# Performance work log

Measured on AMD Instinct MI355X. Metric: run time of the kernel, lower is better.

## Reference

```python
import jax, jax.numpy as jnp
import numpy as np

E = 64        # num_local_experts
N = 32768     # total permuted tokens
H = 1024      # hidden_dim
F = 1024      # intermediate_dim
C = N // E    # per-expert capacity (setup uses equal token counts)


def setup_inputs() -> dict:
    key = jax.random.key(0)
    k1, k2, k3, k4 = jax.random.split(key, 4)
    s = 0.02  # init scale
    return {
        "permuted_local_hidden_states": jax.random.normal(k1, (N, H), jnp.float32),
        "tokens_per_expert": jnp.full((E,), C, dtype=jnp.int32),
        "w_gate": jax.random.normal(k2, (E, H, F), jnp.float32) * s,
        "w_up": jax.random.normal(k3, (E, H, F), jnp.float32) * s,
        "w_down": jax.random.normal(k4, (E, F, H), jnp.float32) * s,
    }


def reference(permuted_local_hidden_states, tokens_per_expert, w_gate, w_up, w_down):
    x = permuted_local_hidden_states  # [N, H], sorted by expert
    counts = tokens_per_expert.astype(jnp.int32)  # [E]
    # start offset of each expert's contiguous token range (torch cumsum + cat([0]))
    starts = jnp.concatenate([jnp.zeros((1,), jnp.int32), jnp.cumsum(counts)])[:-1]
    # expert id and within-expert position for every token (jit-friendly dispatch)
    eid = jnp.repeat(jnp.arange(E, dtype=jnp.int32), counts, total_repeat_length=N)
    pos = jnp.arange(N, dtype=jnp.int32) - starts[eid]
    # gather tokens into fixed-capacity per-expert buffer [E, C, H]; unused slots stay 0
    buf = jnp.zeros((E, C, H), x.dtype).at[eid, pos].set(x)
    # grouped LLaMA MLP: down( silu(gate(x)) * up(x) ), one GEMM triple per expert, batched
    gate = jnp.einsum('ech,ehf->ecf', buf, w_gate)
    up = jnp.einsum('ech,ehf->ecf', buf, w_up)
    h = jax.nn.silu(gate) * up                      # [E, C, F]
    out_buf = jnp.einsum('ecf,efh->ech', h, w_down)  # [E, C, H]
    # scatter back to flat token order (output_local[start:end] = output)
    output_local = out_buf[eid, pos]  # [N, H]
    return output_local
```

## Files before the change

kernel.cpp:

```cpp
#include <hip/hip_runtime.h>
#include <stdint.h>


#define NUM_E 64
#define DIM_H 1024
#define DIM_F 1024
#define CAP   512

typedef short short8 __attribute__((ext_vector_type(8)));
typedef float f32x4 __attribute__((ext_vector_type(4)));

__device__ __forceinline__ uint32_t cvtpk(float lo, float hi) {
  uint32_t r;
  asm("v_cvt_pk_bf16_f32 %0, %1, %2" : "=v"(r) : "v"(lo), "v"(hi));
  return r;
}
__device__ __forceinline__ unsigned short f2bf(float a) {
  uint32_t ua = __builtin_bit_cast(uint32_t, a);
  ua += 0x7FFFu + ((ua >> 16) & 1u);
  return (unsigned short)(ua >> 16);
}
__device__ __forceinline__ void gload_lds16(const void* g, void* l) {
  __builtin_amdgcn_global_load_lds((const __attribute__((address_space(1))) uint32_t*)g,
                                   (__attribute__((address_space(3))) uint32_t*)l, 16, 0, 0);
}

__global__ __launch_bounds__(256, 2) void gateup_kernel(
    const float* __restrict__ x, const float* __restrict__ wg,
    const float* __restrict__ wu, unsigned short* __restrict__ hout)
{
  __shared__ unsigned char smem[49152];
  const int t = threadIdx.x;
  int bid = blockIdx.x;
  bid = (bid & 7) * 512 + (bid >> 3);
  const int e = bid >> 6, rr = bid & 63, mb = rr >> 4, nb = rr & 15;
  const int row0 = e * CAP + mb * 128;
  const int col0 = nb * 64;
  const float* Ag  = x  + (size_t)row0 * DIM_H;
  const float* Bgg = wg + (size_t)e * (DIM_H * DIM_F) + col0;
  const float* Bug = wu + (size_t)e * (DIM_H * DIM_F) + col0;

  const int lane = t & 63, wid = t >> 6;
  const int wm = wid >> 1, wn = wid & 1;

  f32x4 acc[4][4];
  #pragma unroll
  for (int i = 0; i < 4; i++)
    #pragma unroll
    for (int j = 0; j < 4; j++) acc[i][j] = f32x4{0.f, 0.f, 0.f, 0.f};

  const int bn = t & 63, bkb = (t >> 6) * 4;
  float bg[16], bu[16];

  auto loadB = [&](int k0) {
    #pragma unroll
    for (int it = 0; it < 4; it++) {
      int ks = bkb + it * 16;
      #pragma unroll
      for (int i = 0; i < 4; i++) {
        bg[it*4+i] = Bgg[(size_t)(k0 + ks + i) * DIM_F + bn];
        bu[it*4+i] = Bug[(size_t)(k0 + ks + i) * DIM_F + bn];
      }
    }
  };
  auto writeB = [&]() {
    #pragma unroll
    for (int it = 0; it < 4; it++) {
      int ks = bkb + it * 16;
      int off = 32768 + bn * 128 + ((ks * 2) ^ ((bn & 7) << 4));
      *reinterpret_cast<uint2*>(&smem[off]) =
          make_uint2(cvtpk(bg[it*4+0], bg[it*4+1]), cvtpk(bg[it*4+2], bg[it*4+3]));
      *reinterpret_cast<uint2*>(&smem[off + 8192]) =
          make_uint2(cvtpk(bu[it*4+0], bu[it*4+1]), cvtpk(bu[it*4+2], bu[it*4+3]));
    }
  };
  auto loadA = [&](int k0) {
    #pragma unroll
    for (int j = 0; j < 8; j++) {
      int lin = (wid * 8 + j) * 1024 + lane * 16;
      int r = lin >> 8;
      int q = (lin >> 4) & 15;
      const void* src = (const unsigned char*)Ag + (size_t)r * 4096 + k0 * 4 + ((q ^ (r & 7)) * 16);
      gload_lds16(src, &smem[(wid * 8 + j) * 1024]);
    }
  };
  auto ldA = [&](int mi, int kk) -> short8 {
    int r = wm * 64 + mi * 16 + (lane & 15);
    int c = kk * 128 + (lane >> 4) * 32;
    int swz = (r & 7) << 4;
    f32x4 f0 = *reinterpret_cast<const f32x4*>(&smem[r * 256 + (c ^ swz)]);
    f32x4 f1 = *reinterpret_cast<const f32x4*>(&smem[r * 256 + ((c + 16) ^ swz)]);
    int4 ai = make_int4((int)cvtpk(f0[0], f0[1]), (int)cvtpk(f0[2], f0[3]),
                        (int)cvtpk(f1[0], f1[1]), (int)cvtpk(f1[2], f1[3]));
    return __builtin_bit_cast(short8, ai);
  };
  auto ldB = [&](int base, int n, int kk) -> short8 {
    int off = base + n * 128 + ((kk * 64 + (lane >> 4) * 16) ^ ((n & 7) << 4));
    return *reinterpret_cast<const short8*>(&smem[off]);
  };
  auto compute = [&]() {
    #pragma unroll
    for (int kk = 0; kk < 2; kk++) {
      short8 a[4], bgf[2], buf_[2];
      #pragma unroll
      for (int mi = 0; mi < 4; mi++) a[mi] = ldA(mi, kk);
      #pragma unroll
      for (int ni = 0; ni < 2; ni++) {
        int n = wn * 32 + ni * 16 + (lane & 15);
        bgf[ni]  = ldB(32768, n, kk);
        buf_[ni] = ldB(40960, n, kk);
      }
      #pragma unroll
      for (int mi = 0; mi < 4; mi++)
        #pragma unroll
        for (int ni = 0; ni < 2; ni++) {
          acc[mi][ni]     = __builtin_amdgcn_mfma_f32_16x16x32_bf16(a[mi], bgf[ni],  acc[mi][ni],     0, 0, 0);
          acc[mi][ni + 2] = __builtin_amdgcn_mfma_f32_16x16x32_bf16(a[mi], buf_[ni], acc[mi][ni + 2], 0, 0, 0);
        }
    }
  };

  loadB(0);
  loadA(0);
  writeB();
  __syncthreads();
  const int NT = DIM_H / 64;
  for (int kt = 0; kt < NT; kt++) {
    if (kt + 1 < NT) loadB((kt + 1) * 64);
    compute();
    __syncthreads();
    if (kt + 1 < NT) { loadA((kt + 1) * 64); writeB(); __syncthreads(); }
  }

  #pragma unroll
  for (int mi = 0; mi < 4; mi++)
    #pragma unroll
    for (int nc = 0; nc < 2; nc++) {
      int col = col0 + wn * 32 + nc * 16 + (lane & 15);
      int rbase = row0 + wm * 64 + mi * 16 + (lane >> 4) * 4;
      #pragma unroll
      for (int j = 0; j < 4; j++) {
        float g = acc[mi][nc][j], u = acc[mi][nc + 2][j];
        float hv = (g / (1.f + __expf(-g))) * u;
        hout[(size_t)(rbase + j) * DIM_F + col] = f2bf(hv);
      }
    }
}

__global__ __launch_bounds__(256, 2) void down_kernel(
    const unsigned short* __restrict__ hin, const float* __restrict__ wd,
    float* __restrict__ out)
{
  __shared__ unsigned char smem[32768];
  const int t = threadIdx.x;
  int bid = blockIdx.x;
  bid = (bid & 7) * 256 + (bid >> 3);
  const int e = bid >> 5, rr = bid & 31, mb = rr >> 3, nb = rr & 7;
  const int row0 = e * CAP + mb * 128;
  const int col0 = nb * 128;
  const unsigned short* Ag = hin + (size_t)row0 * DIM_F;
  const float* Bdg = wd + (size_t)e * (DIM_F * DIM_H) + col0;

  const int lane = t & 63, wid = t >> 6;
  const int wm = wid >> 1, wn = wid & 1;

  f32x4 acc[4][4];
  #pragma unroll
  for (int i = 0; i < 4; i++)
    #pragma unroll
    for (int j = 0; j < 4; j++) acc[i][j] = f32x4{0.f, 0.f, 0.f, 0.f};

  const int bn = t & 127, bkb = (t >> 7) * 4;
  float bs[32];

  auto loadB = [&](int k0) {
    #pragma unroll
    for (int it = 0; it < 8; it++) {
      int ks = bkb + it * 8;
      #pragma unroll
      for (int i = 0; i < 4; i++)
        bs[it*4+i] = Bdg[(size_t)(k0 + ks + i) * DIM_H + bn];
    }
  };
  auto writeB = [&]() {
    #pragma unroll
    for (int it = 0; it < 8; it++) {
      int ks = bkb + it * 8;
      int off = 16384 + bn * 128 + ((ks * 2) ^ ((bn & 7) << 4));
      *reinterpret_cast<uint2*>(&smem[off]) =
          make_uint2(cvtpk(bs[it*4+0], bs[it*4+1]), cvtpk(bs[it*4+2], bs[it*4+3]));
    }
  };
  auto loadA = [&](int k0) {
    #pragma unroll
    for (int j = 0; j < 4; j++) {
      int lin = (wid * 4 + j) * 1024 + lane * 16;
      int r = lin >> 7;
      int q = (lin >> 4) & 7;
      const void* src = (const unsigned char*)Ag + (size_t)r * 2048 + k0 * 2 + ((q ^ (r & 7)) * 16);
      gload_lds16(src, &smem[(wid * 4 + j) * 1024]);
    }
  };
  auto ldA = [&](int mi, int kk) -> short8 {
    int r = wm * 64 + mi * 16 + (lane & 15);
    int off = r * 128 + ((kk * 64 + (lane >> 4) * 16) ^ ((r & 7) << 4));
    return *reinterpret_cast<const short8*>(&smem[off]);
  };
  auto ldB = [&](int ni, int kk) -> short8 {
    int n = wn * 64 + ni * 16 + (lane & 15);
    int off = 16384 + n * 128 + ((kk * 64 + (lane >> 4) * 16) ^ ((n & 7) << 4));
    return *reinterpret_cast<const short8*>(&smem[off]);
  };
  auto compute = [&]() {
    #pragma unroll
    for (int kk = 0; kk < 2; kk++) {
      short8 a[4], b[4];
      #pragma unroll
      for (int mi = 0; mi < 4; mi++) a[mi] = ldA(mi, kk);
      #pragma unroll
      for (int ni = 0; ni < 4; ni++) b[ni] = ldB(ni, kk);
      #pragma unroll
      for (int mi = 0; mi < 4; mi++)
        #pragma unroll
        for (int ni = 0; ni < 4; ni++)
          acc[mi][ni] = __builtin_amdgcn_mfma_f32_16x16x32_bf16(a[mi], b[ni], acc[mi][ni], 0, 0, 0);
    }
  };

  loadB(0);
  loadA(0);
  writeB();
  __syncthreads();
  const int NT = DIM_F / 64;
  for (int kt = 0; kt < NT; kt++) {
    if (kt + 1 < NT) loadB((kt + 1) * 64);
    compute();
    __syncthreads();
    if (kt + 1 < NT) { loadA((kt + 1) * 64); writeB(); __syncthreads(); }
  }

  #pragma unroll
  for (int mi = 0; mi < 4; mi++)
    #pragma unroll
    for (int ni = 0; ni < 4; ni++) {
      int col = col0 + wn * 64 + ni * 16 + (lane & 15);
      int rbase = row0 + wm * 64 + mi * 16 + (lane >> 4) * 4;
      #pragma unroll
      for (int j = 0; j < 4; j++)
        out[(size_t)(rbase + j) * DIM_H + col] = acc[mi][ni][j];
    }
}

extern "C" void kernel_launch(void* const* d_in, const int* in_sizes, int n_in,
                              void* d_out, int out_size, void* d_ws, size_t ws_size,
                              hipStream_t stream) {
  (void)in_sizes; (void)n_in; (void)out_size; (void)ws_size;
  const float* x  = (const float*)d_in[0];
  const float* wg = (const float*)d_in[2];
  const float* wu = (const float*)d_in[3];
  const float* wd = (const float*)d_in[4];
  unsigned short* h = (unsigned short*)d_ws;
  float* out = (float*)d_out;

  gateup_kernel<<<dim3(4096), dim3(256), 0, stream>>>(x, wg, wu, h);
  down_kernel<<<dim3(2048), dim3(256), 0, stream>>>(h, wd, out);
}
```

Baseline: 448.8 us.

## Pre-convert activations to bf16 and multi-buffer LDS pipeline in both GEMMs

Adds a separate pass that converts the fp32 token activations to bf16 in workspace, so the gate/up kernel can stream A tiles straight into LDS with direct global-to-LDS loads. Both GEMM kernels switch to a triple-buffered A and double-buffered B pipeline in 80KB of LDS, with explicit vmcnt waits, sched barriers, one barrier per k-step and raised priority during the MFMA sections. The goal is to overlap global loads with compute and cut barrier stalls. The costs are an extra kernel launch and a full read/write of x, plus larger LDS use that may limit how many blocks fit per CU. The fallback path is only taken when the workspace is too small.

```diff
diff --git a/kernel.cpp b/kernel.cpp
--- a/kernel.cpp
+++ b/kernel.cpp
@@ -6,9 +6,15 @@
 #define DIM_H 1024
 #define DIM_F 1024
 #define CAP   512
+#define NTOK  32768
 
 typedef short short8 __attribute__((ext_vector_type(8)));
 typedef float f32x4 __attribute__((ext_vector_type(4)));
+
+#define VMCNT(n)  asm volatile("s_waitcnt vmcnt(" #n ")" ::: "memory")
+#define LGKMCNT0  asm volatile("s_waitcnt lgkmcnt(0)" ::: "memory")
+#define SBAR      __builtin_amdgcn_s_barrier()
+#define SCHED0    __builtin_amdgcn_sched_barrier(0)
 
 __device__ __forceinline__ uint32_t cvtpk(float lo, float hi) {
   uint32_t r;
@@ -23,6 +29,151 @@
 __device__ __forceinline__ void gload_lds16(const void* g, void* l) {
   __builtin_amdgcn_global_load_lds((const __attribute__((address_space(1))) uint32_t*)g,
                                    (__attribute__((address_space(3))) uint32_t*)l, 16, 0, 0);
+}
+
+__global__ __launch_bounds__(256) void cvt_kernel(const float* __restrict__ x,
+                                                  unsigned short* __restrict__ xbf) {
+  size_t i = ((size_t)blockIdx.x * 256 + threadIdx.x) * 8;
+  f32x4 a = *reinterpret_cast<const f32x4*>(x + i);
+  f32x4 b = *reinterpret_cast<const f32x4*>(x + i + 4);
+  int4 o = make_int4((int)cvtpk(a[0], a[1]), (int)cvtpk(a[2], a[3]),
+                     (int)cvtpk(b[0], b[1]), (int)cvtpk(b[2], b[3]));
+  *reinterpret_cast<int4*>(xbf + i) = o;
+}
+
+__global__ __launch_bounds__(256, 2) void gateup_kernel_bf(
+    const unsigned short* __restrict__ xbf, const float* __restrict__ wg,
+    const float* __restrict__ wu, unsigned short* __restrict__ hout)
+{
+  __shared__ unsigned char smem[81920];
+  const int t = threadIdx.x;
+  int bid = blockIdx.x;
+  bid = (bid & 7) * 512 + (bid >> 3);
+  const int e = bid >> 6, rr = bid & 63, mb = rr >> 4, nb = rr & 15;
+  const int row0 = e * CAP + mb * 128;
+  const int col0 = nb * 64;
+  const unsigned short* Ag = xbf + (size_t)row0 * DIM_H;
+  const float* Bgg = wg + (size_t)e * (DIM_H * DIM_F) + col0;
+  const float* Bug = wu + (size_t)e * (DIM_H * DIM_F) + col0;
+
+  const int lane = t & 63, wid = t >> 6;
+  const int wm = wid >> 1, wn = wid & 1;
+
+  f32x4 acc[4][4];
+  #pragma unroll
+  for (int i = 0; i < 4; i++)
+    #pragma unroll
+    for (int j = 0; j < 4; j++) acc[i][j] = f32x4{0.f, 0.f, 0.f, 0.f};
+
+  const int bn = t & 63, bkb = (t >> 6) * 4;
+  float bg[16], bu[16];
+
+  auto loadB = [&](int k0) {
+    #pragma unroll
+    for (int it = 0; it < 4; it++) {
+      int ks = bkb + it * 16;
+      #pragma unroll
+      for (int i = 0; i < 4; i++) {
+        bg[it*4+i] = Bgg[(size_t)(k0 + ks + i) * DIM_F + bn];
+        bu[it*4+i] = Bug[(size_t)(k0 + ks + i) * DIM_F + bn];
+      }
+    }
+  };
+  auto writeB = [&](int b) {
+    const int Bb = 49152 + b * 16384;
+    #pragma unroll
+    for (int it = 0; it < 4; it++) {
+      int ks = bkb + it * 16;
+      int off = Bb + bn * 128 + ((ks * 2) ^ ((bn & 7) << 4));
+      *reinterpret_cast<uint2*>(&smem[off]) =
+          make_uint2(cvtpk(bg[it*4+0], bg[it*4+1]), cvtpk(bg[it*4+2], bg[it*4+3]));
+      *reinterpret_cast<uint2*>(&smem[off + 8192]) =
+          make_uint2(cvtpk(bu[it*4+0], bu[it*4+1]), cvtpk(bu[it*4+2], bu[it*4+3]));
+    }
+  };
+  auto loadA = [&](int k0, int buf) {
+    #pragma unroll
+    for (int j = 0; j < 4; j++) {
+      int lin = (wid * 4 + j) * 1024 + lane * 16;
+      int r = lin >> 7;
+      int q = (lin >> 4) & 7;
+      const void* src = (const unsigned char*)Ag + (size_t)r * 2048 + k0 * 2 + ((q ^ (r & 7)) * 16);
+      gload_lds16(src, &smem[buf * 16384 + (wid * 4 + j) * 1024]);
+    }
+  };
+  auto compute = [&](int kt) {
+    const int Ab = (kt % 3) * 16384;
+    const int Bb = 49152 + (kt & 1) * 16384;
+    __builtin_amdgcn_s_setprio(1);
+    #pragma unroll
+    for (int kk = 0; kk < 2; kk++) {
+      short8 a[4], bgf[2], buf_[2];
+      #pragma unroll
+      for (int mi = 0; mi < 4; mi++) {
+        int r = wm * 64 + mi * 16 + (lane & 15);
+        a[mi] = *reinterpret_cast<const short8*>(
+            &smem[Ab + r * 128 + ((kk * 64 + (lane >> 4) * 16) ^ ((r & 7) << 4))]);
+      }
+      #pragma unroll
+      for (int ni = 0; ni < 2; ni++) {
+        int n = wn * 32 + ni * 16 + (lane & 15);
+        int off = Bb + n * 128 + ((kk * 64 + (lane >> 4) * 16) ^ ((n & 7) << 4));
+        bgf[ni]  = *reinterpret_cast<const short8*>(&smem[off]);
+        buf_[ni] = *reinterpret_cast<const short8*>(&smem[off + 8192]);
+      }
+      #pragma unroll
+      for (int mi = 0; mi < 4; mi++)
+        #pragma unroll
+        for (int ni = 0; ni < 2; ni++) {
+          acc[mi][ni]     = __builtin_amdgcn_mfma_f32_16x16x32_bf16(a[mi], bgf[ni],  acc[mi][ni],     0, 0, 0);
+          acc[mi][ni + 2] = __builtin_amdgcn_mfma_f32_16x16x32_bf16(a[mi], buf_[ni], acc[mi][ni + 2], 0, 0, 0);
+        }
+    }
+    __builtin_amdgcn_s_setprio(0);
+  };
+
+  const int NT = DIM_H / 64;
+  loadB(0);
+  loadA(0, 0);
+  loadA(64, 1);
+  SCHED0;
+  VMCNT(8);
+  SCHED0;
+  writeB(0);
+  VMCNT(4);
+  LGKMCNT0;
+  SCHED0;
+  SBAR;
+  for (int kt = 0; kt < NT; kt++) {
+    if (kt + 1 < NT) {
+      loadB((kt + 1) * 64);
+      if (kt + 2 < NT) loadA((kt + 2) * 64, (kt + 2) % 3);
+      SCHED0;
+    }
+    compute(kt);
+    if (kt + 1 < NT) {
+      if (kt + 2 < NT) { VMCNT(4); } else { VMCNT(0); }
+      SCHED0;
+      writeB((kt + 1) & 1);
+      LGKMCNT0;
+      SCHED0;
+      SBAR;
+    }
+  }
+
+  #pragma unroll
+  for (int mi = 0; mi < 4; mi++)
+    #pragma unroll
+    for (int nc = 0; nc < 2; nc++) {
+      int col = col0 + wn * 32 + nc * 16 + (lane & 15);
+      int rbase = row0 + wm * 64 + mi * 16 + (lane >> 4) * 4;
+      #pragma unroll
+      for (int j = 0; j < 4; j++) {
+        float g = acc[mi][nc][j], u = acc[mi][nc + 2][j];
+        float hv = (g / (1.f + __expf(-g))) * u;
+        hout[(size_t)(rbase + j) * DIM_F + col] = f2bf(hv);
+      }
+    }
 }
 
 __global__ __launch_bounds__(256, 2) void gateup_kernel(
@@ -39,19 +190,15 @@
   const float* Ag  = x  + (size_t)row0 * DIM_H;
   const float* Bgg = wg + (size_t)e * (DIM_H * DIM_F) + col0;
   const float* Bug = wu + (size_t)e * (DIM_H * DIM_F) + col0;
-
   const int lane = t & 63, wid = t >> 6;
   const int wm = wid >> 1, wn = wid & 1;
-
   f32x4 acc[4][4];
   #pragma unroll
   for (int i = 0; i < 4; i++)
     #pragma unroll
     for (int j = 0; j < 4; j++) acc[i][j] = f32x4{0.f, 0.f, 0.f, 0.f};
-
   const int bn = t & 63, bkb = (t >> 6) * 4;
   float bg[16], bu[16];
-
   auto loadB = [&](int k0) {
     #pragma unroll
     for (int it = 0; it < 4; it++) {
@@ -119,7 +266,6 @@
         }
     }
   };
-
   loadB(0);
   loadA(0);
   writeB();
@@ -131,7 +277,6 @@
     __syncthreads();
     if (kt + 1 < NT) { loadA((kt + 1) * 64); writeB(); __syncthreads(); }
   }
-
   #pragma unroll
   for (int mi = 0; mi < 4; mi++)
     #pragma unroll
@@ -151,7 +296,7 @@
     const unsigned short* __restrict__ hin, const float* __restrict__ wd,
     float* __restrict__ out)
 {
-  __shared__ unsigned char smem[32768];
+  __shared__ unsigned char smem[81920];
   const int t = threadIdx.x;
   int bid = blockIdx.x;
   bid = (bid & 7) * 256 + (bid >> 3);
@@ -182,61 +327,81 @@
         bs[it*4+i] = Bdg[(size_t)(k0 + ks + i) * DIM_H + bn];
     }
   };
-  auto writeB = [&]() {
+  auto writeB = [&](int b) {
+    const int Bb = 49152 + b * 16384;
     #pragma unroll
     for (int it = 0; it < 8; it++) {
       int ks = bkb + it * 8;
-      int off = 16384 + bn * 128 + ((ks * 2) ^ ((bn & 7) << 4));
+      int off = Bb + bn * 128 + ((ks * 2) ^ ((bn & 7) << 4));
       *reinterpret_cast<uint2*>(&smem[off]) =
           make_uint2(cvtpk(bs[it*4+0], bs[it*4+1]), cvtpk(bs[it*4+2], bs[it*4+3]));
     }
   };
-  auto loadA = [&](int k0) {
+  auto loadA = [&](int k0, int buf) {
     #pragma unroll
     for (int j = 0; j < 4; j++) {
       int lin = (wid * 4 + j) * 1024 + lane * 16;
       int r = lin >> 7;
       int q = (lin >> 4) & 7;
       const void* src = (const unsigned char*)Ag + (size_t)r * 2048 + k0 * 2 + ((q ^ (r & 7)) * 16);
-      gload_lds16(src, &smem[(wid * 4 + j) * 1024]);
-    }
-  };
-  auto ldA = [&](int mi, int kk) -> short8 {
-    int r = wm * 64 + mi * 16 + (lane & 15);
-    int off = r * 128 + ((kk * 64 + (lane >> 4) * 16) ^ ((r & 7) << 4));
-    return *reinterpret_cast<const short8*>(&smem[off]);
-  };
-  auto ldB = [&](int ni, int kk) -> short8 {
-    int n = wn * 64 + ni * 16 + (lane & 15);
-    int off = 16384 + n * 128 + ((kk * 64 + (lane >> 4) * 16) ^ ((n & 7) << 4));
-    return *reinterpret_cast<const short8*>(&smem[off]);
-  };
-  auto compute = [&]() {
+      gload_lds16(src, &smem[buf * 16384 + (wid * 4 + j) * 1024]);
+    }
+  };
+  auto compute = [&](int kt) {
+    const int Ab = (kt % 3) * 16384;
+    const int Bb = 49152 + (kt & 1) * 16384;
+    __builtin_amdgcn_s_setprio(1);
     #pragma unroll
     for (int kk = 0; kk < 2; kk++) {
       short8 a[4], b[4];
       #pragma unroll
-      for (int mi = 0; mi < 4; mi++) a[mi] = ldA(mi, kk);
-      #pragma unroll
-      for (int ni = 0; ni < 4; ni++) b[ni] = ldB(ni, kk);
+      for (int mi = 0; mi < 4; mi++) {
+        int r = wm * 64 + mi * 16 + (lane & 15);
+        a[mi] = *reinterpret_cast<const short8*>(
+            &smem[Ab + r * 128 + ((kk * 64 + (lane >> 4) * 16) ^ ((r & 7) << 4))]);
+      }
+      #pragma unroll
+      for (int ni = 0; ni < 4; ni++) {
+        int n = wn * 64 + ni * 16 + (lane & 15);
+        b[ni] = *reinterpret_cast<const short8*>(
+            &smem[Bb + n * 128 + ((kk * 64 + (lane >> 4) * 16) ^ ((n & 7) << 4))]);
+      }
       #pragma unroll
       for (int mi = 0; mi < 4; mi++)
         #pragma unroll
         for (int ni = 0; ni < 4; ni++)
           acc[mi][ni] = __builtin_amdgcn_mfma_f32_16x16x32_bf16(a[mi], b[ni], acc[mi][ni], 0, 0, 0);
     }
-  };
-
+    __builtin_amdgcn_s_setprio(0);
+  };
+
+  const int NT = DIM_F / 64;
   loadB(0);
-  loadA(0);
-  writeB();
-  __syncthreads();
-  const int NT = DIM_F / 64;
+  loadA(0, 0);
+  loadA(64, 1);
+  SCHED0;
+  VMCNT(8);
+  SCHED0;
+  writeB(0);
+  VMCNT(4);
+  LGKMCNT0;
+  SCHED0;
+  SBAR;
   for (int kt = 0; kt < NT; kt++) {
-    if (kt + 1 < NT) loadB((kt + 1) * 64);
-    compute();
-    __syncthreads();
-    if (kt + 1 < NT) { loadA((kt + 1) * 64); writeB(); __syncthreads(); }
+    if (kt + 1 < NT) {
+      loadB((kt + 1) * 64);
+      if (kt + 2 < NT) loadA((kt + 2) * 64, (kt + 2) % 3);
+      SCHED0;
+    }
+    compute(kt);
+    if (kt + 1 < NT) {
+      if (kt + 2 < NT) { VMCNT(4); } else { VMCNT(0); }
+      SCHED0;
+      writeB((kt + 1) & 1);
+      LGKMCNT0;
+      SCHED0;
+      SBAR;
+    }
   }
 
   #pragma unroll
@@ -254,14 +419,21 @@
 extern "C" void kernel_launch(void* const* d_in, const int* in_sizes, int n_in,
                               void* d_out, int out_size, void* d_ws, size_t ws_size,
                               hipStream_t stream) {
-  (void)in_sizes; (void)n_in; (void)out_size; (void)ws_size;
+  (void)in_sizes; (void)n_in; (void)out_size;
   const float* x  = (const float*)d_in[0];
   const float* wg = (const float*)d_in[2];
   const float* wu = (const float*)d_in[3];
   const float* wd = (const float*)d_in[4];
   unsigned short* h = (unsigned short*)d_ws;
+  const size_t h_bytes = (size_t)NTOK * DIM_F * 2;
   float* out = (float*)d_out;
 
-  gateup_kernel<<<dim3(4096), dim3(256), 0, stream>>>(x, wg, wu, h);
+  if (ws_size >= h_bytes + (size_t)NTOK * DIM_H * 2) {
+    unsigned short* xbf = (unsigned short*)((char*)d_ws + h_bytes);
+    cvt_kernel<<<dim3((NTOK * DIM_H) / (256 * 8)), dim3(256), 0, stream>>>(x, xbf);
+    gateup_kernel_bf<<<dim3(4096), dim3(256), 0, stream>>>(xbf, wg, wu, h);
+  } else {
+    gateup_kernel<<<dim3(4096), dim3(256), 0, stream>>>(x, wg, wu, h);
+  }
   down_kernel<<<dim3(2048), dim3(256), 0, stream>>>(h, wd, out);
 }
```

New measurement: 426.7 us. 1.05x faster.

## Pre-convert activations to bf16 and enlarge double-buffered GEMM tiles

Applied to the files above, without the earlier changes.

Adds a separate kernel that converts the fp32 token activations to bf16 once, so the GEMM kernels no longer convert A tiles inside the inner loop. Both grouped GEMMs move to 512-thread blocks with 256x128 output tiles. This halves the number of times each expert's fp32 weights are re-read across row blocks. The kernels also double-buffer A and B in LDS with explicit vmcnt/lgkmcnt waits and a single barrier per k-step, and raise wave priority around the MFMA section. The cost is much larger LDS use per block (up to 128 KB), which limits occupancy, plus an extra pass over the activations and extra workspace.

```diff
diff --git a/kernel.cpp b/kernel.cpp
--- a/kernel.cpp
+++ b/kernel.cpp
@@ -6,9 +6,15 @@
 #define DIM_H 1024
 #define DIM_F 1024
 #define CAP   512
+#define NTOK  32768
 
 typedef short short8 __attribute__((ext_vector_type(8)));
 typedef float f32x4 __attribute__((ext_vector_type(4)));
+
+#define VMCNT(n)  asm volatile("s_waitcnt vmcnt(" #n ")" ::: "memory")
+#define LGKMCNT0  asm volatile("s_waitcnt lgkmcnt(0)" ::: "memory")
+#define SBAR      __builtin_amdgcn_s_barrier()
+#define SCHED0    __builtin_amdgcn_sched_barrier(0)
 
 __device__ __forceinline__ uint32_t cvtpk(float lo, float hi) {
   uint32_t r;
@@ -25,138 +31,152 @@
                                    (__attribute__((address_space(3))) uint32_t*)l, 16, 0, 0);
 }
 
-__global__ __launch_bounds__(256, 2) void gateup_kernel(
-    const float* __restrict__ x, const float* __restrict__ wg,
+__global__ __launch_bounds__(256) void cvt_kernel(const float* __restrict__ x,
+                                                  unsigned short* __restrict__ xbf) {
+  size_t i = ((size_t)blockIdx.x * 256 + threadIdx.x) * 8;
+  f32x4 a = *reinterpret_cast<const f32x4*>(x + i);
+  f32x4 b = *reinterpret_cast<const f32x4*>(x + i + 4);
+  int4 o = make_int4((int)cvtpk(a[0], a[1]), (int)cvtpk(a[2], a[3]),
+                     (int)cvtpk(b[0], b[1]), (int)cvtpk(b[2], b[3]));
+  *reinterpret_cast<int4*>(xbf + i) = o;
+}
+
+__global__ __launch_bounds__(512, 2) void gateup_kernel_v3(
+    const unsigned short* __restrict__ xbf, const float* __restrict__ wg,
     const float* __restrict__ wu, unsigned short* __restrict__ hout)
 {
-  __shared__ unsigned char smem[49152];
+  __shared__ unsigned char smem[131072];
   const int t = threadIdx.x;
   int bid = blockIdx.x;
-  bid = (bid & 7) * 512 + (bid >> 3);
-  const int e = bid >> 6, rr = bid & 63, mb = rr >> 4, nb = rr & 15;
-  const int row0 = e * CAP + mb * 128;
-  const int col0 = nb * 64;
-  const float* Ag  = x  + (size_t)row0 * DIM_H;
+  bid = (bid & 7) * 128 + (bid >> 3);
+  const int e = bid >> 4, rr = bid & 15, mb = rr >> 3, nb = rr & 7;
+  const int row0 = e * CAP + mb * 256;
+  const int col0 = nb * 128;
+  const unsigned short* Ag = xbf + (size_t)row0 * DIM_H;
   const float* Bgg = wg + (size_t)e * (DIM_H * DIM_F) + col0;
   const float* Bug = wu + (size_t)e * (DIM_H * DIM_F) + col0;
 
   const int lane = t & 63, wid = t >> 6;
   const int wm = wid >> 1, wn = wid & 1;
 
-  f32x4 acc[4][4];
+  f32x4 accg[4][4], accu[4][4];
   #pragma unroll
   for (int i = 0; i < 4; i++)
     #pragma unroll
-    for (int j = 0; j < 4; j++) acc[i][j] = f32x4{0.f, 0.f, 0.f, 0.f};
-
-  const int bn = t & 63, bkb = (t >> 6) * 4;
+    for (int j = 0; j < 4; j++) {
+      accg[i][j] = f32x4{0.f, 0.f, 0.f, 0.f};
+      accu[i][j] = f32x4{0.f, 0.f, 0.f, 0.f};
+    }
+
+  const int bn = t & 127, bkb = (t >> 7) * 16;
   float bg[16], bu[16];
 
   auto loadB = [&](int k0) {
     #pragma unroll
-    for (int it = 0; it < 4; it++) {
-      int ks = bkb + it * 16;
-      #pragma unroll
-      for (int i = 0; i < 4; i++) {
-        bg[it*4+i] = Bgg[(size_t)(k0 + ks + i) * DIM_F + bn];
-        bu[it*4+i] = Bug[(size_t)(k0 + ks + i) * DIM_F + bn];
-      }
-    }
-  };
-  auto writeB = [&]() {
-    #pragma unroll
-    for (int it = 0; it < 4; it++) {
-      int ks = bkb + it * 16;
-      int off = 32768 + bn * 128 + ((ks * 2) ^ ((bn & 7) << 4));
+    for (int i = 0; i < 16; i++) {
+      bg[i] = Bgg[(size_t)(k0 + bkb + i) * DIM_F + bn];
+      bu[i] = Bug[(size_t)(k0 + bkb + i) * DIM_F + bn];
+    }
+  };
+  auto writeB = [&](int b) {
+    const int Bb = 65536 + b * 32768;
+    #pragma unroll
+    for (int j = 0; j < 4; j++) {
+      int off = Bb + bn * 128 + (((bkb + j * 4) * 2) ^ ((bn & 7) << 4));
       *reinterpret_cast<uint2*>(&smem[off]) =
-          make_uint2(cvtpk(bg[it*4+0], bg[it*4+1]), cvtpk(bg[it*4+2], bg[it*4+3]));
-      *reinterpret_cast<uint2*>(&smem[off + 8192]) =
-          make_uint2(cvtpk(bu[it*4+0], bu[it*4+1]), cvtpk(bu[it*4+2], bu[it*4+3]));
-    }
-  };
-  auto loadA = [&](int k0) {
-    #pragma unroll
-    for (int j = 0; j < 8; j++) {
-      int lin = (wid * 8 + j) * 1024 + lane * 16;
-      int r = lin >> 8;
-      int q = (lin >> 4) & 15;
-      const void* src = (const unsigned char*)Ag + (size_t)r * 4096 + k0 * 4 + ((q ^ (r & 7)) * 16);
-      gload_lds16(src, &smem[(wid * 8 + j) * 1024]);
-    }
-  };
-  auto ldA = [&](int mi, int kk) -> short8 {
-    int r = wm * 64 + mi * 16 + (lane & 15);
-    int c = kk * 128 + (lane >> 4) * 32;
-    int swz = (r & 7) << 4;
-    f32x4 f0 = *reinterpret_cast<const f32x4*>(&smem[r * 256 + (c ^ swz)]);
-    f32x4 f1 = *reinterpret_cast<const f32x4*>(&smem[r * 256 + ((c + 16) ^ swz)]);
-    int4 ai = make_int4((int)cvtpk(f0[0], f0[1]), (int)cvtpk(f0[2], f0[3]),
-                        (int)cvtpk(f1[0], f1[1]), (int)cvtpk(f1[2], f1[3]));
-    return __builtin_bit_cast(short8, ai);
-  };
-  auto ldB = [&](int base, int n, int kk) -> short8 {
-    int off = base + n * 128 + ((kk * 64 + (lane >> 4) * 16) ^ ((n & 7) << 4));
-    return *reinterpret_cast<const short8*>(&smem[off]);
-  };
-  auto compute = [&]() {
+          make_uint2(cvtpk(bg[j*4+0], bg[j*4+1]), cvtpk(bg[j*4+2], bg[j*4+3]));
+      *reinterpret_cast<uint2*>(&smem[off + 16384]) =
+          make_uint2(cvtpk(bu[j*4+0], bu[j*4+1]), cvtpk(bu[j*4+2], bu[j*4+3]));
+    }
+  };
+  auto loadA = [&](int k0, int buf) {
+    #pragma unroll
+    for (int j = 0; j < 4; j++) {
+      int lin = (j * 512 + t) * 16;
+      int r = lin >> 7;
+      int q = (lin >> 4) & 7;
+      const void* src = (const unsigned char*)Ag + (size_t)r * 2048 + k0 * 2 + ((q ^ (r & 7)) * 16);
+      gload_lds16(src, &smem[buf * 32768 + lin]);
+    }
+  };
+  auto compute = [&](int kt) {
+    const int Ab = (kt & 1) * 32768;
+    const int Bb = 65536 + (kt & 1) * 32768;
+    __builtin_amdgcn_s_setprio(1);
     #pragma unroll
     for (int kk = 0; kk < 2; kk++) {
-      short8 a[4], bgf[2], buf_[2];
-      #pragma unroll
-      for (int mi = 0; mi < 4; mi++) a[mi] = ldA(mi, kk);
-      #pragma unroll
-      for (int ni = 0; ni < 2; ni++) {
-        int n = wn * 32 + ni * 16 + (lane & 15);
-        bgf[ni]  = ldB(32768, n, kk);
-        buf_[ni] = ldB(40960, n, kk);
+      short8 a[4], bgf[4], buf_[4];
+      #pragma unroll
+      for (int mi = 0; mi < 4; mi++) {
+        int r = wm * 64 + mi * 16 + (lane & 15);
+        a[mi] = *reinterpret_cast<const short8*>(
+            &smem[Ab + r * 128 + ((kk * 64 + (lane >> 4) * 16) ^ ((r & 7) << 4))]);
+      }
+      #pragma unroll
+      for (int ni = 0; ni < 4; ni++) {
+        int n = wn * 64 + ni * 16 + (lane & 15);
+        int off = Bb + n * 128 + ((kk * 64 + (lane >> 4) * 16) ^ ((n & 7) << 4));
+        bgf[ni]  = *reinterpret_cast<const short8*>(&smem[off]);
+        buf_[ni] = *reinterpret_cast<const short8*>(&smem[off + 16384]);
       }
       #pragma unroll
       for (int mi = 0; mi < 4; mi++)
         #pragma unroll
-        for (int ni = 0; ni < 2; ni++) {
-          acc[mi][ni]     = __builtin_amdgcn_mfma_f32_16x16x32_bf16(a[mi], bgf[ni],  acc[mi][ni],     0, 0, 0);
-          acc[mi][ni + 2] = __builtin_amdgcn_mfma_f32_16x16x32_bf16(a[mi], buf_[ni], acc[mi][ni + 2], 0, 0, 0);
+        for (int ni = 0; ni < 4; ni++) {
+          accg[mi][ni] = __builtin_amdgcn_mfma_f32_16x16x32_bf16(a[mi], bgf[ni],  accg[mi][ni], 0, 0, 0);
+          accu[mi][ni] = __builtin_amdgcn_mfma_f32_16x16x32_bf16(a[mi], buf_[ni], accu[mi][ni], 0, 0, 0);
         }
     }
-  };
-
+    __builtin_amdgcn_s_setprio(0);
+  };
+
+  const int NT = DIM_H / 64;
   loadB(0);
-  loadA(0);
-  writeB();
-  __syncthreads();
-  const int NT = DIM_H / 64;
+  loadA(0, 0);
+  VMCNT(4); SCHED0;
+  writeB(0);
+  LGKMCNT0; VMCNT(0); SCHED0;
+  SBAR;
   for (int kt = 0; kt < NT; kt++) {
-    if (kt + 1 < NT) loadB((kt + 1) * 64);
-    compute();
-    __syncthreads();
-    if (kt + 1 < NT) { loadA((kt + 1) * 64); writeB(); __syncthreads(); }
+    if (kt + 1 < NT) {
+      loadB((kt + 1) * 64);
+      loadA((kt + 1) * 64, (kt + 1) & 1);
+      SCHED0;
+    }
+    compute(kt);
+    if (kt + 1 < NT) {
+      VMCNT(4); SCHED0;
+      writeB((kt + 1) & 1);
+      LGKMCNT0; VMCNT(0); SCHED0;
+      SBAR;
+    }
   }
 
   #pragma unroll
   for (int mi = 0; mi < 4; mi++)
     #pragma unroll
-    for (int nc = 0; nc < 2; nc++) {
-      int col = col0 + wn * 32 + nc * 16 + (lane & 15);
+    for (int ni = 0; ni < 4; ni++) {
+      int col = col0 + wn * 64 + ni * 16 + (lane & 15);
       int rbase = row0 + wm * 64 + mi * 16 + (lane >> 4) * 4;
       #pragma unroll
       for (int j = 0; j < 4; j++) {
-        float g = acc[mi][nc][j], u = acc[mi][nc + 2][j];
+        float g = accg[mi][ni][j], u = accu[mi][ni][j];
         float hv = (g / (1.f + __expf(-g))) * u;
         hout[(size_t)(rbase + j) * DIM_F + col] = f2bf(hv);
       }
     }
 }
 
-__global__ __launch_bounds__(256, 2) void down_kernel(
+__global__ __launch_bounds__(512, 2) void down_kernel_v3(
     const unsigned short* __restrict__ hin, const float* __restrict__ wd,
     float* __restrict__ out)
 {
-  __shared__ unsigned char smem[32768];
+  __shared__ unsigned char smem[98304];
   const int t = threadIdx.x;
   int bid = blockIdx.x;
-  bid = (bid & 7) * 256 + (bid >> 3);
-  const int e = bid >> 5, rr = bid & 31, mb = rr >> 3, nb = rr & 7;
-  const int row0 = e * CAP + mb * 128;
+  bid = (bid & 7) * 128 + (bid >> 3);
+  const int e = bid >> 4, rr = bid & 15, mb = rr >> 3, nb = rr & 7;
+  const int row0 = e * CAP + mb * 256;
   const int col0 = nb * 128;
   const unsigned short* Ag = hin + (size_t)row0 * DIM_F;
   const float* Bdg = wd + (size_t)e * (DIM_F * DIM_H) + col0;
@@ -170,73 +190,81 @@
     #pragma unroll
     for (int j = 0; j < 4; j++) acc[i][j] = f32x4{0.f, 0.f, 0.f, 0.f};
 
-  const int bn = t & 127, bkb = (t >> 7) * 4;
-  float bs[32];
+  const int bn = t & 127, bkb = (t >> 7) * 16;
+  float bs[16];
 
   auto loadB = [&](int k0) {
     #pragma unroll
-    for (int it = 0; it < 8; it++) {
-      int ks = bkb + it * 8;
-      #pragma unroll
-      for (int i = 0; i < 4; i++)
-        bs[it*4+i] = Bdg[(size_t)(k0 + ks + i) * DIM_H + bn];
-    }
-  };
-  auto writeB = [&]() {
-    #pragma unroll
-    for (int it = 0; it < 8; it++) {
-      int ks = bkb + it * 8;
-      int off = 16384 + bn * 128 + ((ks * 2) ^ ((bn & 7) << 4));
+    for (int i = 0; i < 16; i++)
+      bs[i] = Bdg[(size_t)(k0 + bkb + i) * DIM_H + bn];
+  };
+  auto writeB = [&](int b) {
+    const int Bb = 65536 + b * 16384;
+    #pragma unroll
+    for (int j = 0; j < 4; j++) {
+      int off = Bb + bn * 128 + (((bkb + j * 4) * 2) ^ ((bn & 7) << 4));
       *reinterpret_cast<uint2*>(&smem[off]) =
-          make_uint2(cvtpk(bs[it*4+0], bs[it*4+1]), cvtpk(bs[it*4+2], bs[it*4+3]));
-    }
-  };
-  auto loadA = [&](int k0) {
-    #pragma unroll
-    for (int j = 0; j < 4; j++) {
-      int lin = (wid * 4 + j) * 1024 + lane * 16;
+          make_uint2(cvtpk(bs[j*4+0], bs[j*4+1]), cvtpk(bs[j*4+2], bs[j*4+3]));
+    }
+  };
+  auto loadA = [&](int k0, int buf) {
+    #pragma unroll
+    for (int j = 0; j < 4; j++) {
+      int lin = (j * 512 + t) * 16;
       int r = lin >> 7;
       int q = (lin >> 4) & 7;
       const void* src = (const unsigned char*)Ag + (size_t)r * 2048 + k0 * 2 + ((q ^ (r & 7)) * 16);
-      gload_lds16(src, &smem[(wid * 4 + j) * 1024]);
-    }
-  };
-  auto ldA = [&](int mi, int kk) -> short8 {
-    int r = wm * 64 + mi * 16 + (lane & 15);
-    int off = r * 128 + ((kk * 64 + (lane >> 4) * 16) ^ ((r & 7) << 4));
-    return *reinterpret_cast<const short8*>(&smem[off]);
-  };
-  auto ldB = [&](int ni, int kk) -> short8 {
-    int n = wn * 64 + ni * 16 + (lane & 15);
-    int off = 16384 + n * 128 + ((kk * 64 + (lane >> 4) * 16) ^ ((n & 7) << 4));
-    return *reinterpret_cast<const short8*>(&smem[off]);
-  };
-  auto compute = [&]() {
+      gload_lds16(src, &smem[buf * 32768 + lin]);
+    }
+  };
+  auto compute = [&](int kt) {
+    const int Ab = (kt & 1) * 32768;
+    const int Bb = 65536 + (kt & 1) * 16384;
+    __builtin_amdgcn_s_setprio(1);
     #pragma unroll
     for (int kk = 0; kk < 2; kk++) {
       short8 a[4], b[4];
       #pragma unroll
-      for (int mi = 0; mi < 4; mi++) a[mi] = ldA(mi, kk);
-      #pragma unroll
-      for (int ni = 0; ni < 4; ni++) b[ni] = ldB(ni, kk);
+      for (int mi = 0; mi < 4; mi++) {
+        int r = wm * 64 + mi * 16 + (lane & 15);
+        a[mi] = *reinterpret_cast<const short8*>(
+            &smem[Ab + r * 128 + ((kk * 64 + (lane >> 4) * 16) ^ ((r & 7) << 4))]);
+      }
+      #pragma unroll
+      for (int ni = 0; ni < 4; ni++) {
+        int n = wn * 64 + ni * 16 + (lane & 15);
+        b[ni] = *reinterpret_cast<const short8*>(
+            &smem[Bb + n * 128 + ((kk * 64 + (lane >> 4) * 16) ^ ((n & 7) << 4))]);
+      }
       #pragma unroll
       for (int mi = 0; mi < 4; mi++)
         #pragma unroll
         for (int ni = 0; ni < 4; ni++)
           acc[mi][ni] = __builtin_amdgcn_mfma_f32_16x16x32_bf16(a[mi], b[ni], acc[mi][ni], 0, 0, 0);
     }
-  };
-
+    __builtin_amdgcn_s_setprio(0);
+  };
+
+  const int NT = DIM_F / 64;
   loadB(0);
-  loadA(0);
-  writeB();
-  __syncthreads();
-  const int NT = DIM_F / 64;
+  loadA(0, 0);
+  VMCNT(4); SCHED0;
+  writeB(0);
+  LGKMCNT0; VMCNT(0); SCHED0;
+  SBAR;
   for (int kt = 0; kt < NT; kt++) {
-    if (kt + 1 < NT) loadB((kt + 1) * 64);
-    compute();
-    __syncthreads();
-    if (kt + 1 < NT) { loadA((kt + 1) * 64); writeB(); __syncthreads(); }
+    if (kt + 1 < NT) {
+      loadB((kt + 1) * 64);
+      loadA((kt + 1) * 64, (kt + 1) & 1);
+      SCHED0;
+    }
+    compute(kt);
+    if (kt + 1 < NT) {
+      VMCNT(4); SCHED0;
+      writeB((kt + 1) & 1);
+      LGKMCNT0; VMCNT(0); SCHED0;
+      SBAR;
+    }
   }
 
   #pragma unroll
@@ -259,9 +287,11 @@
   const float* wg = (const float*)d_in[2];
   const float* wu = (const float*)d_in[3];
   const float* wd = (const float*)d_in[4];
-  unsigned short* h = (unsigned short*)d_ws;
+  unsigned short* h   = (unsigned short*)d_ws;
+  unsigned short* xbf = (unsigned short*)((char*)d_ws + (size_t)NTOK * DIM_F * 2);
   float* out = (float*)d_out;
 
-  gateup_kernel<<<dim3(4096), dim3(256), 0, stream>>>(x, wg, wu, h);
-  down_kernel<<<dim3(2048), dim3(256), 0, stream>>>(h, wd, out);
-}
+  cvt_kernel<<<dim3((NTOK * DIM_H) / (256 * 8)), dim3(256), 0, stream>>>(x, xbf);
+  gateup_kernel_v3<<<dim3(1024), dim3(512), 0, stream>>>(xbf, wg, wu, h);
+  down_kernel_v3<<<dim3(1024), dim3(512), 0, stream>>>(h, wd, out);
+}
```

Measured after the change: 365.2 us. 18.6% less time.
